# Optimization experiments

Hardware: AMD Instinct MI355X
Metric: run time of the kernel (lower is better)

Reference implementation:

```python
import jax, jax.numpy as jnp
import numpy as np

K = 3          # kernel size
STRIDE = 1
PAD = 1
DIL = 1


def setup_inputs() -> dict:
    key = jax.random.key(0)
    k1, k2, k3 = jax.random.split(key, 3)
    N, Cin, H, W = 8, 128, 64, 64
    Cout = 128
    x = jax.random.normal(k1, (N, Cin, H, W), dtype=jnp.float32)
    # offset channels: 2 * deformable_groups * K*K = 18, interleaved (dy, dx) per tap
    offset = jax.random.normal(k2, (N, 2 * K * K, H, W), dtype=jnp.float32)
    weight = jax.random.normal(k3, (Cout, Cin, K, K), dtype=jnp.float32) / np.sqrt(Cin * K * K)
    return {"x": x, "offset": offset, "weight": weight}


def _deform_conv(x, offset, weight):
    N, Cin, H, W = x.shape
    Cout = weight.shape[0]
    KK = K * K
    Ho, Wo = offset.shape[2], offset.shape[3]

    off = offset.reshape(N, KK, 2, Ho, Wo)
    dy = off[:, :, 0]  # [N, KK, Ho, Wo]
    dx = off[:, :, 1]

    kh = jnp.repeat(jnp.arange(K), K).astype(x.dtype)   # [KK]
    kw = jnp.tile(jnp.arange(K), K).astype(x.dtype)     # [KK]
    base_i = (jnp.arange(Ho) * STRIDE - PAD).astype(x.dtype)  # [Ho]
    base_j = (jnp.arange(Wo) * STRIDE - PAD).astype(x.dtype)  # [Wo]

    # Sampling positions: [N, KK, Ho, Wo]
    py = base_i[None, None, :, None] + (kh * DIL)[None, :, None, None] + dy
    px = base_j[None, None, None, :] + (kw * DIL)[None, :, None, None] + dx

    y0 = jnp.floor(py)
    x0 = jnp.floor(px)
    wy1 = py - y0
    wx1 = px - x0
    wy0 = 1.0 - wy1
    wx0 = 1.0 - wx1
    y0i = y0.astype(jnp.int32)
    x0i = x0.astype(jnp.int32)
    y1i = y0i + 1
    x1i = x0i + 1

    x_flat = x.reshape(N, Cin, H * W)

    def gather(yi, xi):
        # zero-padding outside the image
        mask = ((yi >= 0) & (yi < H) & (xi >= 0) & (xi < W)).astype(x.dtype)
        idx = jnp.clip(yi, 0, H - 1) * W + jnp.clip(xi, 0, W - 1)  # [N,KK,Ho,Wo]
        v = jnp.take_along_axis(x_flat, idx.reshape(N, 1, -1), axis=2)  # [N,Cin,KK*Ho*Wo]
        v = v.reshape(N, Cin, KK, Ho, Wo)
        return v * mask[:, None]

    sampled = (gather(y0i, x0i) * (wy0 * wx0)[:, None]
               + gather(y0i, x1i) * (wy0 * wx1)[:, None]
               + gather(y1i, x0i) * (wy1 * wx0)[:, None]
               + gather(y1i, x1i) * (wy1 * wx1)[:, None])  # [N,Cin,KK,Ho,Wo]

    w = weight.reshape(Cout, Cin, KK)
    return jnp.einsum('nckij,ock->noij', sampled, w)


def reference(x, offset, weight):
    return _deform_conv(x, offset, weight)
```

## Files before the change

kernel.cpp:

```cpp
#include <hip/hip_runtime.h>


#define H  64
#define W  64
#define CIN 128
#define COUT 128
#define NB 8
#define KK 9
#define SROW (CIN + 8)

typedef short bf16x8 __attribute__((ext_vector_type(8)));
typedef float f32x4  __attribute__((ext_vector_type(4)));

__device__ __forceinline__ unsigned short f2bf(float f) {
    unsigned u = __builtin_bit_cast(unsigned, f);
    u += 0x7FFFu + ((u >> 16) & 1u);
    return (unsigned short)(u >> 16);
}
__device__ __forceinline__ unsigned cvt_pk_bf16(float lo, float hi) {
    unsigned r;
    asm("v_cvt_pk_bf16_f32 %0, %1, %2" : "=v"(r) : "v"(lo), "v"(hi));
    return r;
}
__device__ __forceinline__ float lo_f(unsigned u) { return __builtin_bit_cast(float, u << 16); }
__device__ __forceinline__ float hi_f(unsigned u) { return __builtin_bit_cast(float, u & 0xFFFF0000u); }

__global__ void prep_all(const float* __restrict__ x, const float* __restrict__ w,
                         unsigned short* __restrict__ xt, unsigned short* __restrict__ wt) {
    int b = blockIdx.x;
    int t = threadIdx.x;
    if (b >= NB * H) {
        int idx = (b - NB * H) * 256 + t;
        if (idx < KK * COUT * CIN) {
            int e  = idx & 7;
            int lq = (idx >> 3) & 3;
            int lm = (idx >> 5) & 15;
            int ct = (idx >> 9) & 3;
            int nt = (idx >> 11) & 1;
            int c4 = (idx >> 12) & 3;
            int kk = idx >> 14;
            int co = (c4 << 5) + (nt << 4) + lm;
            int ch = (ct << 5) + (lq << 3) + e;
            wt[idx] = f2bf(w[(co * CIN + ch) * KK + kk]);
        }
        return;
    }
    __shared__ float tile[CIN][W + 4];
    int n = b & 7, y = b >> 3;
    const float* src = x + ((size_t)n * CIN * H + y) * W;
    #pragma unroll
    for (int it = 0; it < 8; ++it) {
        int idx = it * 256 + t;
        int c  = idx >> 4;
        int x4 = (idx & 15) << 2;
        int xs = (x4 + ((c >> 5) << 4)) & 63;
        *(float4*)&tile[c][xs] = *(const float4*)(src + (size_t)c * H * W + x4);
    }
    __syncthreads();
    int xp = t >> 2;
    int cbch = (t & 3) << 5;
    int xr = (xp + ((cbch >> 5) << 4)) & 63;
    unsigned short* dst = xt + (((size_t)(n * H + y) * W + xp) * CIN + cbch);
    unsigned rr[16];
    #pragma unroll
    for (int i = 0; i < 16; ++i)
        rr[i] = cvt_pk_bf16(tile[cbch + 2 * i][xr], tile[cbch + 2 * i + 1][xr]);
    #pragma unroll
    for (int i = 0; i < 4; ++i)
        ((uint4*)dst)[i] = make_uint4(rr[4*i], rr[4*i+1], rr[4*i+2], rr[4*i+3]);
}

struct GatherCtx {
    const unsigned short *c00, *c01, *c10, *c11;
    float w00, w01, w10, w11;
};

__device__ __forceinline__ GatherCtx gather_setup(float dy, float dx, int ho, int wo, int kk,
                                                  const unsigned short* xbase) {
    GatherCtx g;
    float py = (float)(ho - 1 + kk / 3) + dy;
    float px = (float)(wo - 1 + kk % 3) + dx;
    float y0f = floorf(py), x0f = floorf(px);
    float wy1 = py - y0f, wx1 = px - x0f;
    float wy0 = 1.f - wy1, wx0 = 1.f - wx1;
    int y0 = (int)y0f, x0 = (int)x0f;
    int y1 = y0 + 1, x1 = x0 + 1;
    bool vy0 = (unsigned)y0 < (unsigned)H, vy1 = (unsigned)y1 < (unsigned)H;
    bool vx0 = (unsigned)x0 < (unsigned)W, vx1 = (unsigned)x1 < (unsigned)W;
    g.w00 = (vy0 && vx0) ? wy0 * wx0 : 0.f;
    g.w01 = (vy0 && vx1) ? wy0 * wx1 : 0.f;
    g.w10 = (vy1 && vx0) ? wy1 * wx0 : 0.f;
    g.w11 = (vy1 && vx1) ? wy1 * wx1 : 0.f;
    int yc0 = min(max(y0, 0), H - 1), yc1 = min(max(y1, 0), H - 1);
    int xc0 = min(max(x0, 0), W - 1), xc1 = min(max(x1, 0), W - 1);
    const unsigned short* r0 = xbase + (size_t)yc0 * W * CIN;
    const unsigned short* r1 = xbase + (size_t)yc1 * W * CIN;
    g.c00 = r0 + xc0 * CIN;  g.c01 = r0 + xc1 * CIN;
    g.c10 = r1 + xc0 * CIN;  g.c11 = r1 + xc1 * CIN;
    return g;
}

__device__ __forceinline__ void gather_issue(const GatherCtx& g, uint4* gv) {
    #pragma unroll
    for (int j = 0; j < 4; ++j) {
        gv[4*j+0] = *(const uint4*)(g.c00 + 8*j);
        gv[4*j+1] = *(const uint4*)(g.c01 + 8*j);
        gv[4*j+2] = *(const uint4*)(g.c10 + 8*j);
        gv[4*j+3] = *(const uint4*)(g.c11 + 8*j);
    }
}

__device__ __forceinline__ void gather_blend_store(const GatherCtx& g, const uint4* gv,
                                                   unsigned short* dst) {
    #pragma unroll
    for (int j = 0; j < 4; ++j) {
        const unsigned* a0 = (const unsigned*)&gv[4*j+0];
        const unsigned* a1 = (const unsigned*)&gv[4*j+1];
        const unsigned* a2 = (const unsigned*)&gv[4*j+2];
        const unsigned* a3 = (const unsigned*)&gv[4*j+3];
        unsigned rr[4];
        #pragma unroll
        for (int i = 0; i < 4; ++i) {
            float v0 = g.w00*lo_f(a0[i]) + g.w01*lo_f(a1[i]) + g.w10*lo_f(a2[i]) + g.w11*lo_f(a3[i]);
            float v1 = g.w00*hi_f(a0[i]) + g.w01*hi_f(a1[i]) + g.w10*hi_f(a2[i]) + g.w11*hi_f(a3[i]);
            rr[i] = cvt_pk_bf16(v0, v1);
        }
        *(uint4*)(dst + 8*j) = make_uint4(rr[0], rr[1], rr[2], rr[3]);
    }
}

__global__ __launch_bounds__(512, 4) void deform_main(
        const float* __restrict__ offs, const unsigned short* __restrict__ xt,
        const unsigned short* __restrict__ wt, float* __restrict__ out) {
    __shared__ __attribute__((aligned(16))) unsigned short samp[2][64][SROW];

    int b = blockIdx.x;
    int n = b & 7, ho = b >> 3;
    int t = threadIdx.x;
    int lane = t & 63, wv = t >> 6;
    bool producer = (wv >= 4);

    if (producer) {
        int t2 = t - 256;
        int p  = t2 >> 2;
        int cb = (t2 & 3) << 5;
        const float* offbase = offs + (size_t)n * 2 * KK * H * W + (size_t)ho * W + p;
        const unsigned short* xbase = xt + (size_t)n * H * W * CIN + cb;

        float dyA = offbase[0];
        float dxA = offbase[(size_t)H * W];
        {
            GatherCtx g = gather_setup(dyA, dxA, ho, p, 0, xbase);
            uint4 gv[16];
            gather_issue(g, gv);
            dyA = offbase[(size_t)2 * H * W];
            dxA = offbase[(size_t)3 * H * W];
            gather_blend_store(g, gv, &samp[0][p][cb]);
        }
        __syncthreads();
        for (int k = 0; k < KK; ++k) {
            if (k < KK - 1) {
                int tap = k + 1;
                GatherCtx g = gather_setup(dyA, dxA, ho, p, tap, xbase);
                uint4 gv[16];
                gather_issue(g, gv);
                if (k < KK - 2) {
                    dyA = offbase[(size_t)(2 * (tap + 1)) * H * W];
                    dxA = offbase[(size_t)(2 * (tap + 1) + 1) * H * W];
                }
                gather_blend_store(g, gv, &samp[tap & 1][p][cb]);
            }
            __syncthreads();
        }
        return;
    }

    int lm = lane & 15, lq = lane >> 4;
    int cobase = wv << 5;
    int slot = (lm << 2) + lq;

    f32x4 acc[4][2];
    #pragma unroll
    for (int mt = 0; mt < 4; ++mt)
        #pragma unroll
        for (int nt = 0; nt < 2; ++nt) acc[mt][nt] = f32x4{0.f, 0.f, 0.f, 0.f};

    const unsigned short* wvbase = wt + ((size_t)wv << 12) + (slot << 3);

    __syncthreads();
    for (int k = 0; k < KK; ++k) {
        const unsigned short* wkb = wvbase + ((size_t)(k << 2) << 12);
        bf16x8 bW[2][4];
        #pragma unroll
        for (int nt = 0; nt < 2; ++nt)
            #pragma unroll
            for (int ct = 0; ct < 4; ++ct)
                bW[nt][ct] = *(const bf16x8*)(wkb + (((nt << 2) + ct) << 9));

        __builtin_amdgcn_s_setprio(1);
        #pragma unroll
        for (int ct = 0; ct < 4; ++ct) {
            bf16x8 a[4];
            #pragma unroll
            for (int mt = 0; mt < 4; ++mt)
                a[mt] = *(const bf16x8*)&samp[k & 1][lm + (mt << 4)][(ct << 5) + (lq << 3)];
            #pragma unroll
            for (int mt = 0; mt < 4; ++mt) {
                acc[mt][0] = __builtin_amdgcn_mfma_f32_16x16x32_bf16(a[mt], bW[0][ct], acc[mt][0], 0, 0, 0);
                acc[mt][1] = __builtin_amdgcn_mfma_f32_16x16x32_bf16(a[mt], bW[1][ct], acc[mt][1], 0, 0, 0);
            }
        }
        __builtin_amdgcn_s_setprio(0);
        __syncthreads();
    }

    #pragma unroll
    for (int mt = 0; mt < 4; ++mt) {
        int wob = (mt << 4) + (lq << 2);
        #pragma unroll
        for (int nt = 0; nt < 2; ++nt) {
            int co = cobase + (nt << 4) + lm;
            *(f32x4*)(out + (((size_t)(n * COUT + co) * H + ho) * W + wob)) = acc[mt][nt];
        }
    }
}

extern "C" void kernel_launch(void* const* d_in, const int* in_sizes, int n_in,
                              void* d_out, int out_size, void* d_ws, size_t ws_size,
                              hipStream_t stream) {
    const float* x      = (const float*)d_in[0];
    const float* offset = (const float*)d_in[1];
    const float* weight = (const float*)d_in[2];
    float* out = (float*)d_out;

    unsigned short* xt = (unsigned short*)d_ws;
    unsigned short* wt = (unsigned short*)((char*)d_ws + (size_t)NB*H*W*CIN*2);

    int wblocks = (KK * COUT * CIN + 255) / 256;
    hipLaunchKernelGGL(prep_all, dim3(NB * H + wblocks), dim3(256), 0, stream,
                       x, weight, xt, wt);
    hipLaunchKernelGGL(deform_main, dim3(NB * H), dim3(512), 0, stream,
                       offset, xt, wt, out);
}
```

Measured before the change: 111.0 us.

## Replace block barriers with LDS flag handshakes and triple-buffer sampled tiles

Producer and consumer waves now coordinate through per-tap shared-memory ready/done counters with spin-waits, replacing the block-wide __syncthreads after every tap. The sample buffer grows from double to triple buffering so producers can run up to three taps ahead of the MFMA consumers. Weight loads become inline-asm global loads issued before the spin-wait so they overlap with it. The cost is extra LDS, atomic traffic and spinning, and possible ordering hazards from the manual waitcnt placement.

After: 108.2 us. -2.5%, faster.

```diff
diff --git a/kernel.cpp b/kernel.cpp
--- a/kernel.cpp
+++ b/kernel.cpp
@@ -11,6 +11,9 @@
 
 typedef short bf16x8 __attribute__((ext_vector_type(8)));
 typedef float f32x4  __attribute__((ext_vector_type(4)));
+
+#define GLOADX4(dst, ptr) \
+    asm volatile("global_load_dwordx4 %0, %1, off" : "=v"(dst) : "v"(ptr))
 
 __device__ __forceinline__ unsigned short f2bf(float f) {
     unsigned u = __builtin_bit_cast(unsigned, f);
@@ -110,37 +113,38 @@
     }
 }
 
-__device__ __forceinline__ void gather_blend_store(const GatherCtx& g, const uint4* gv,
-                                                   unsigned short* dst) {
+__device__ __forceinline__ void gather_blend(const GatherCtx& g, const uint4* gv, unsigned* rr) {
     #pragma unroll
     for (int j = 0; j < 4; ++j) {
         const unsigned* a0 = (const unsigned*)&gv[4*j+0];
         const unsigned* a1 = (const unsigned*)&gv[4*j+1];
         const unsigned* a2 = (const unsigned*)&gv[4*j+2];
         const unsigned* a3 = (const unsigned*)&gv[4*j+3];
-        unsigned rr[4];
         #pragma unroll
         for (int i = 0; i < 4; ++i) {
             float v0 = g.w00*lo_f(a0[i]) + g.w01*lo_f(a1[i]) + g.w10*lo_f(a2[i]) + g.w11*lo_f(a3[i]);
             float v1 = g.w00*hi_f(a0[i]) + g.w01*hi_f(a1[i]) + g.w10*hi_f(a2[i]) + g.w11*hi_f(a3[i]);
-            rr[i] = cvt_pk_bf16(v0, v1);
-        }
-        *(uint4*)(dst + 8*j) = make_uint4(rr[0], rr[1], rr[2], rr[3]);
+            rr[4*j+i] = cvt_pk_bf16(v0, v1);
+        }
     }
 }
 
 __global__ __launch_bounds__(512, 4) void deform_main(
         const float* __restrict__ offs, const unsigned short* __restrict__ xt,
         const unsigned short* __restrict__ wt, float* __restrict__ out) {
-    __shared__ __attribute__((aligned(16))) unsigned short samp[2][64][SROW];
+    __shared__ __attribute__((aligned(16))) unsigned short samp[3][64][SROW];
+    __shared__ int rdy[KK];
+    __shared__ int dn[KK];
 
     int b = blockIdx.x;
     int n = b & 7, ho = b >> 3;
     int t = threadIdx.x;
     int lane = t & 63, wv = t >> 6;
-    bool producer = (wv >= 4);
-
-    if (producer) {
+
+    if (t < KK) { rdy[t] = 0; dn[t] = 0; }
+    __syncthreads();
+
+    if (wv >= 4) {
         int t2 = t - 256;
         int p  = t2 >> 2;
         int cb = (t2 & 3) << 5;
@@ -149,28 +153,28 @@
 
         float dyA = offbase[0];
         float dxA = offbase[(size_t)H * W];
-        {
-            GatherCtx g = gather_setup(dyA, dxA, ho, p, 0, xbase);
+        #pragma unroll
+        for (int tap = 0; tap < KK; ++tap) {
+            GatherCtx g = gather_setup(dyA, dxA, ho, p, tap, xbase);
             uint4 gv[16];
             gather_issue(g, gv);
-            dyA = offbase[(size_t)2 * H * W];
-            dxA = offbase[(size_t)3 * H * W];
-            gather_blend_store(g, gv, &samp[0][p][cb]);
-        }
-        __syncthreads();
-        for (int k = 0; k < KK; ++k) {
-            if (k < KK - 1) {
-                int tap = k + 1;
-                GatherCtx g = gather_setup(dyA, dxA, ho, p, tap, xbase);
-                uint4 gv[16];
-                gather_issue(g, gv);
-                if (k < KK - 2) {
-                    dyA = offbase[(size_t)(2 * (tap + 1)) * H * W];
-                    dxA = offbase[(size_t)(2 * (tap + 1) + 1) * H * W];
-                }
-                gather_blend_store(g, gv, &samp[tap & 1][p][cb]);
+            if (tap < KK - 1) {
+                dyA = offbase[(size_t)(2 * (tap + 1)) * H * W];
+                dxA = offbase[(size_t)(2 * (tap + 1) + 1) * H * W];
             }
-            __syncthreads();
+            unsigned rr[16];
+            gather_blend(g, gv, rr);
+            if (tap >= 3) {
+                while (__hip_atomic_load(&dn[tap - 3], __ATOMIC_ACQUIRE,
+                                         __HIP_MEMORY_SCOPE_WORKGROUP) < 4)
+                    __builtin_amdgcn_s_sleep(2);
+            }
+            unsigned short* dst = &samp[tap % 3][p][cb];
+            #pragma unroll
+            for (int i = 0; i < 4; ++i)
+                *(uint4*)(dst + 8 * i) = make_uint4(rr[4*i], rr[4*i+1], rr[4*i+2], rr[4*i+3]);
+            asm volatile("s_waitcnt lgkmcnt(0)" ::: "memory");
+            if (lane == 0) atomicAdd(&rdy[tap], 1);
         }
         return;
     }
@@ -187,15 +191,21 @@
 
     const unsigned short* wvbase = wt + ((size_t)wv << 12) + (slot << 3);
 
-    __syncthreads();
-    for (int k = 0; k < KK; ++k) {
-        const unsigned short* wkb = wvbase + ((size_t)(k << 2) << 12);
+    #pragma unroll
+    for (int tap = 0; tap < KK; ++tap) {
+        const unsigned short* wkb = wvbase + ((size_t)(tap << 2) << 12);
         bf16x8 bW[2][4];
         #pragma unroll
         for (int nt = 0; nt < 2; ++nt)
             #pragma unroll
             for (int ct = 0; ct < 4; ++ct)
-                bW[nt][ct] = *(const bf16x8*)(wkb + (((nt << 2) + ct) << 9));
+                GLOADX4(bW[nt][ct], (wkb + (((nt << 2) + ct) << 9)));
+
+        while (__hip_atomic_load(&rdy[tap], __ATOMIC_ACQUIRE,
+                                 __HIP_MEMORY_SCOPE_WORKGROUP) < 4)
+            __builtin_amdgcn_s_sleep(2);
+        asm volatile("s_waitcnt vmcnt(0)" ::: "memory");
+        __builtin_amdgcn_sched_barrier(0);
 
         __builtin_amdgcn_s_setprio(1);
         #pragma unroll
@@ -203,7 +213,7 @@
             bf16x8 a[4];
             #pragma unroll
             for (int mt = 0; mt < 4; ++mt)
-                a[mt] = *(const bf16x8*)&samp[k & 1][lm + (mt << 4)][(ct << 5) + (lq << 3)];
+                a[mt] = *(const bf16x8*)&samp[tap % 3][lm + (mt << 4)][(ct << 5) + (lq << 3)];
             #pragma unroll
             for (int mt = 0; mt < 4; ++mt) {
                 acc[mt][0] = __builtin_amdgcn_mfma_f32_16x16x32_bf16(a[mt], bW[0][ct], acc[mt][0], 0, 0, 0);
@@ -211,7 +221,9 @@
             }
         }
         __builtin_amdgcn_s_setprio(0);
-        __syncthreads();
+        asm volatile("s_waitcnt lgkmcnt(0)" ::: "memory");
+        __builtin_amdgcn_sched_barrier(0);
+        if (lane == 0) atomicAdd(&dn[tap], 1);
     }
 
     #pragma unroll
```

## Split fused producer/consumer deform kernel into separate sampling and GEMM kernels

Applied to the files above, without the earlier changes.

Replaces the warp-specialized kernel, where producer waves gathered and blended bilinear samples into LDS while consumer waves ran MFMA, with two kernels. The new sampling kernel writes all sampled bf16 columns (N*H*W*9*128) to a workspace buffer using many more blocks. A GEMM kernel then streams those columns through double-buffered LDS. This aims to raise gather parallelism and occupancy, at the cost of a large extra global write and read of the sampled tensor plus one more launch.

Measured after the change: 116.6 us. +5.0%, slower.

```diff
diff --git a/kernel.cpp b/kernel.cpp
--- a/kernel.cpp
+++ b/kernel.cpp
@@ -100,81 +100,60 @@
     return g;
 }
 
-__device__ __forceinline__ void gather_issue(const GatherCtx& g, uint4* gv) {
-    #pragma unroll
-    for (int j = 0; j < 4; ++j) {
+__global__ __launch_bounds__(512, 2) void sample_k(
+        const float* __restrict__ offs, const unsigned short* __restrict__ xt,
+        unsigned short* __restrict__ S) {
+    int b = blockIdx.x;
+    int n = b & 7;
+    int r = b >> 3;
+    int tap = r >> 6;
+    int ho = r & 63;
+    int t = threadIdx.x;
+    int pos = t >> 3;
+    int cb = (t & 7) << 4;
+
+    const float* offp = offs + ((size_t)(n * 2 * KK + 2 * tap) * H + ho) * W + pos;
+    float dy = offp[0];
+    float dx = offp[(size_t)H * W];
+
+    GatherCtx g = gather_setup(dy, dx, ho, pos, tap, xt + (size_t)n * H * W * CIN + cb);
+
+    uint4 gv[8];
+    #pragma unroll
+    for (int j = 0; j < 2; ++j) {
         gv[4*j+0] = *(const uint4*)(g.c00 + 8*j);
         gv[4*j+1] = *(const uint4*)(g.c01 + 8*j);
         gv[4*j+2] = *(const uint4*)(g.c10 + 8*j);
         gv[4*j+3] = *(const uint4*)(g.c11 + 8*j);
     }
-}
-
-__device__ __forceinline__ void gather_blend_store(const GatherCtx& g, const uint4* gv,
-                                                   unsigned short* dst) {
-    #pragma unroll
-    for (int j = 0; j < 4; ++j) {
+    unsigned rr[8];
+    #pragma unroll
+    for (int j = 0; j < 2; ++j) {
         const unsigned* a0 = (const unsigned*)&gv[4*j+0];
         const unsigned* a1 = (const unsigned*)&gv[4*j+1];
         const unsigned* a2 = (const unsigned*)&gv[4*j+2];
         const unsigned* a3 = (const unsigned*)&gv[4*j+3];
-        unsigned rr[4];
         #pragma unroll
         for (int i = 0; i < 4; ++i) {
             float v0 = g.w00*lo_f(a0[i]) + g.w01*lo_f(a1[i]) + g.w10*lo_f(a2[i]) + g.w11*lo_f(a3[i]);
             float v1 = g.w00*hi_f(a0[i]) + g.w01*hi_f(a1[i]) + g.w10*hi_f(a2[i]) + g.w11*hi_f(a3[i]);
-            rr[i] = cvt_pk_bf16(v0, v1);
-        }
-        *(uint4*)(dst + 8*j) = make_uint4(rr[0], rr[1], rr[2], rr[3]);
-    }
-}
-
-__global__ __launch_bounds__(512, 4) void deform_main(
-        const float* __restrict__ offs, const unsigned short* __restrict__ xt,
-        const unsigned short* __restrict__ wt, float* __restrict__ out) {
+            rr[4*j+i] = cvt_pk_bf16(v0, v1);
+        }
+    }
+    size_t so = ((((size_t)(n * H + ho) * W + pos) * KK + tap) << 7) + cb;
+    *(uint4*)(S + so)     = make_uint4(rr[0], rr[1], rr[2], rr[3]);
+    *(uint4*)(S + so + 8) = make_uint4(rr[4], rr[5], rr[6], rr[7]);
+}
+
+__global__ __launch_bounds__(256, 2) void gemm_k(
+        const unsigned short* __restrict__ S, const unsigned short* __restrict__ wt,
+        float* __restrict__ out) {
     __shared__ __attribute__((aligned(16))) unsigned short samp[2][64][SROW];
 
     int b = blockIdx.x;
     int n = b & 7, ho = b >> 3;
     int t = threadIdx.x;
     int lane = t & 63, wv = t >> 6;
-    bool producer = (wv >= 4);
-
-    if (producer) {
-        int t2 = t - 256;
-        int p  = t2 >> 2;
-        int cb = (t2 & 3) << 5;
-        const float* offbase = offs + (size_t)n * 2 * KK * H * W + (size_t)ho * W + p;
-        const unsigned short* xbase = xt + (size_t)n * H * W * CIN + cb;
-
-        float dyA = offbase[0];
-        float dxA = offbase[(size_t)H * W];
-        {
-            GatherCtx g = gather_setup(dyA, dxA, ho, p, 0, xbase);
-            uint4 gv[16];
-            gather_issue(g, gv);
-            dyA = offbase[(size_t)2 * H * W];
-            dxA = offbase[(size_t)3 * H * W];
-            gather_blend_store(g, gv, &samp[0][p][cb]);
-        }
-        __syncthreads();
-        for (int k = 0; k < KK; ++k) {
-            if (k < KK - 1) {
-                int tap = k + 1;
-                GatherCtx g = gather_setup(dyA, dxA, ho, p, tap, xbase);
-                uint4 gv[16];
-                gather_issue(g, gv);
-                if (k < KK - 2) {
-                    dyA = offbase[(size_t)(2 * (tap + 1)) * H * W];
-                    dxA = offbase[(size_t)(2 * (tap + 1) + 1) * H * W];
-                }
-                gather_blend_store(g, gv, &samp[tap & 1][p][cb]);
-            }
-            __syncthreads();
-        }
-        return;
-    }
-
     int lm = lane & 15, lq = lane >> 4;
     int cobase = wv << 5;
     int slot = (lm << 2) + lq;
@@ -185,11 +164,29 @@
         #pragma unroll
         for (int nt = 0; nt < 2; ++nt) acc[mt][nt] = f32x4{0.f, 0.f, 0.f, 0.f};
 
+    int pos = t >> 2;
+    int seg = t & 3;
+    const unsigned short* srow = S + ((((size_t)(n * H + ho) * W + pos) * KK) << 7) + (seg << 5);
     const unsigned short* wvbase = wt + ((size_t)wv << 12) + (slot << 3);
 
+    {
+        uint4 st[4];
+        #pragma unroll
+        for (int i = 0; i < 4; ++i) st[i] = *(const uint4*)(srow + (i << 3));
+        unsigned short* ld = &samp[0][pos][seg << 5];
+        #pragma unroll
+        for (int i = 0; i < 4; ++i) *(uint4*)(ld + (i << 3)) = st[i];
+    }
     __syncthreads();
-    for (int k = 0; k < KK; ++k) {
-        const unsigned short* wkb = wvbase + ((size_t)(k << 2) << 12);
+
+    for (int tap = 0; tap < KK; ++tap) {
+        uint4 nx[4];
+        if (tap < KK - 1) {
+            const unsigned short* sr = srow + ((size_t)(tap + 1) << 7);
+            #pragma unroll
+            for (int i = 0; i < 4; ++i) nx[i] = *(const uint4*)(sr + (i << 3));
+        }
+        const unsigned short* wkb = wvbase + ((size_t)tap << 14);
         bf16x8 bW[2][4];
         #pragma unroll
         for (int nt = 0; nt < 2; ++nt)
@@ -197,20 +194,23 @@
             for (int ct = 0; ct < 4; ++ct)
                 bW[nt][ct] = *(const bf16x8*)(wkb + (((nt << 2) + ct) << 9));
 
-        __builtin_amdgcn_s_setprio(1);
         #pragma unroll
         for (int ct = 0; ct < 4; ++ct) {
             bf16x8 a[4];
             #pragma unroll
             for (int mt = 0; mt < 4; ++mt)
-                a[mt] = *(const bf16x8*)&samp[k & 1][lm + (mt << 4)][(ct << 5) + (lq << 3)];
+                a[mt] = *(const bf16x8*)&samp[tap & 1][lm + (mt << 4)][(ct << 5) + (lq << 3)];
             #pragma unroll
             for (int mt = 0; mt < 4; ++mt) {
                 acc[mt][0] = __builtin_amdgcn_mfma_f32_16x16x32_bf16(a[mt], bW[0][ct], acc[mt][0], 0, 0, 0);
                 acc[mt][1] = __builtin_amdgcn_mfma_f32_16x16x32_bf16(a[mt], bW[1][ct], acc[mt][1], 0, 0, 0);
             }
         }
-        __builtin_amdgcn_s_setprio(0);
+        if (tap < KK - 1) {
+            unsigned short* ld = &samp[(tap + 1) & 1][pos][seg << 5];
+            #pragma unroll
+            for (int i = 0; i < 4; ++i) *(uint4*)(ld + (i << 3)) = nx[i];
+        }
         __syncthreads();
     }
 
@@ -234,11 +234,14 @@
     float* out = (float*)d_out;
 
     unsigned short* xt = (unsigned short*)d_ws;
-    unsigned short* wt = (unsigned short*)((char*)d_ws + (size_t)NB*H*W*CIN*2);
+    unsigned short* wt = (unsigned short*)((char*)d_ws + 8388608);
+    unsigned short* S  = (unsigned short*)((char*)d_ws + 8683520);
 
     int wblocks = (KK * COUT * CIN + 255) / 256;
     hipLaunchKernelGGL(prep_all, dim3(NB * H + wblocks), dim3(256), 0, stream,
                        x, weight, xt, wt);
-    hipLaunchKernelGGL(deform_main, dim3(NB * H), dim3(512), 0, stream,
-                       offset, xt, wt, out);
-}
+    hipLaunchKernelGGL(sample_k, dim3(NB * KK * H), dim3(512), 0, stream,
+                       offset, xt, S);
+    hipLaunchKernelGGL(gemm_k, dim3(NB * H), dim3(256), 0, stream,
+                       S, wt, out);
+}
```
